# Performance work log

Measured on AMD Instinct MI355X. Metric: run time of the kernel, lower is better.

Reference implementation:

```python
import jax, jax.numpy as jnp
import numpy as np

B, D, E, H, T = 16384, 1024, 8, 512, 256
NUM_TASKS = 3  # purchase, quality, price


def setup_inputs() -> dict:
    key = jax.random.key(0)
    ks = jax.random.split(key, 12)
    s_in = 1.0 / np.sqrt(D)
    s_h = 1.0 / np.sqrt(H)
    s_t = 1.0 / np.sqrt(T)
    return {
        "x": jax.random.normal(ks[0], (B, D), dtype=jnp.float32),
        # expert layer 1: [E, D, H], layer 2: [E, H, H]
        "We1": jax.random.uniform(ks[1], (E, D, H), jnp.float32, -s_in, s_in),
        "be1": jax.random.uniform(ks[2], (E, H), jnp.float32, -s_in, s_in),
        "We2": jax.random.uniform(ks[3], (E, H, H), jnp.float32, -s_h, s_h),
        "be2": jax.random.uniform(ks[4], (E, H), jnp.float32, -s_h, s_h),
        # gates (one per task): [T_tasks, D, E]
        "Wg": jax.random.uniform(ks[5], (NUM_TASKS, D, E), jnp.float32, -s_in, s_in),
        "bg": jax.random.uniform(ks[6], (NUM_TASKS, E), jnp.float32, -s_in, s_in),
        # towers: [T_tasks, H, T] then [T_tasks, T, 1]
        "Wt1": jax.random.uniform(ks[7], (NUM_TASKS, H, T), jnp.float32, -s_h, s_h),
        "bt1": jax.random.uniform(ks[8], (NUM_TASKS, T), jnp.float32, -s_h, s_h),
        "Wt2": jax.random.uniform(ks[9], (NUM_TASKS, T, 1), jnp.float32, -s_t, s_t),
        "bt2": jax.random.uniform(ks[10], (NUM_TASKS, 1), jnp.float32, -s_t, s_t),
    }


def reference(x, We1, be1, We2, be2, Wg, bg, Wt1, bt1, Wt2, bt2):
    # Batched expert MLPs (dropout = identity in eval): [B, E, H]
    h1 = jax.nn.relu(jnp.einsum("bd,edh->beh", x, We1) + be1)
    expert_out = jax.nn.relu(jnp.einsum("beh,ehk->bek", h1, We2) + be2)
    # Per-task softmax gates: [T, B, E]
    gates = jax.nn.softmax(jnp.einsum("bd,tde->tbe", x, Wg) + bg[:, None, :], axis=-1)
    # Weighted combine: [T, B, H]
    task_in = jnp.einsum("tbe,beh->tbh", gates, expert_out)
    # Towers: [T, B, 1]
    th = jax.nn.relu(jnp.einsum("tbh,thk->tbk", task_in, Wt1) + bt1[:, None, :])
    preds = jax.nn.sigmoid(jnp.einsum("tbk,tko->tbo", th, Wt2) + bt2[:, None, :])
    return (preds[0], preds[1], preds[2])
```

## Files before the change

kernel.cpp:

```cpp
#include <hip/hip_runtime.h>


#define BM 128
#define BN 128
#define BK 64

typedef __attribute__((ext_vector_type(8))) short short8;
typedef __attribute__((ext_vector_type(4))) float floatx4;
typedef __attribute__((ext_vector_type(4))) unsigned short ushortx4;
typedef __attribute__((ext_vector_type(8))) unsigned short ushortx8;

__device__ __forceinline__ unsigned short f32_to_bf16(float f) {
  unsigned int u = __float_as_uint(f);
  u += 0x7fffu + ((u >> 16) & 1u);
  return (unsigned short)(u >> 16);
}
__device__ __forceinline__ float bf16_to_f32(unsigned short h) {
  return __uint_as_float(((unsigned int)h) << 16);
}

__device__ __forceinline__ void async_cp16(const void* g, void* lds) {
  __builtin_amdgcn_global_load_lds(
      (const __attribute__((address_space(1))) void*)g,
      (__attribute__((address_space(3))) void*)lds, 16, 0, 0);
}

__device__ __forceinline__ void transpose_slice(
    const float* __restrict__ in, unsigned short* __restrict__ out,
    int K, int N, float (*tile)[33]) {
  int n0 = blockIdx.x * 32, k0 = blockIdx.y * 32;
  for (int i = threadIdx.y; i < 32; i += 8)
    tile[i][threadIdx.x] = in[(size_t)(k0 + i) * N + n0 + threadIdx.x];
  __syncthreads();
  for (int i = threadIdx.y; i < 32; i += 8)
    out[(size_t)(n0 + i) * K + k0 + threadIdx.x] = f32_to_bf16(tile[threadIdx.x][i]);
}

__global__ void prep_kernel(const float* __restrict__ We1, const float* __restrict__ We2,
                            const float* __restrict__ Wt1, const float* __restrict__ Wg,
                            unsigned short* __restrict__ W1T, unsigned short* __restrict__ W2T,
                            unsigned short* __restrict__ Wt1T, float* __restrict__ WgT) {
  __shared__ float tile[32][33];
  int z = blockIdx.z;
  if (z < 8) {
    transpose_slice(We1 + (size_t)z * 524288, W1T + (size_t)z * 524288, 1024, 512, tile);
  } else if (z < 16) {
    if (blockIdx.y < 16)
      transpose_slice(We2 + (size_t)(z - 8) * 262144, W2T + (size_t)(z - 8) * 262144, 512, 512, tile);
  } else if (z < 19) {
    if (blockIdx.x < 8 && blockIdx.y < 16)
      transpose_slice(Wt1 + (size_t)(z - 16) * 131072, Wt1T + (size_t)(z - 16) * 131072, 512, 256, tile);
  } else {
    if (blockIdx.x < 16 && blockIdx.y < 6) {
      int idx = (blockIdx.y * 16 + blockIdx.x) * 256 + threadIdx.y * 32 + threadIdx.x;
      int t = idx >> 13, r = idx & 8191, e = r >> 10, d = r & 1023;
      WgT[idx] = Wg[t * 8192 + d * 8 + e];
    }
  }
}

__global__ __launch_bounds__(256) void gates_cvt_kernel(
    const float* __restrict__ x, const float* __restrict__ WgT,
    const float* __restrict__ bg, float* __restrict__ gout,
    unsigned short* __restrict__ xb) {
  int wave = threadIdx.x >> 6, lane = threadIdx.x & 63;
  int b = blockIdx.x * 4 + wave;
  const float* xr = x + (size_t)b * 1024;
  float xv[16];
#pragma unroll
  for (int j = 0; j < 16; j++) xv[j] = xr[lane + 64 * j];
  unsigned short* xbr = xb + (size_t)b * 1024;
#pragma unroll
  for (int j = 0; j < 16; j++) xbr[lane + 64 * j] = f32_to_bf16(xv[j]);
  float mylogit = 0.f;
#pragma unroll
  for (int te = 0; te < 24; te++) {
    const float* w = WgT + te * 1024;
    float a = 0.f;
#pragma unroll
    for (int j = 0; j < 16; j++) a += xv[j] * w[lane + 64 * j];
#pragma unroll
    for (int off = 32; off > 0; off >>= 1) a += __shfl_xor(a, off, 64);
    if (lane == te) mylogit = a;
  }
  if (lane < 24) {
    int t = lane >> 3, e = lane & 7;
    float logit = mylogit + bg[lane];
    float m = logit;
    m = fmaxf(m, __shfl_xor(m, 4, 64));
    m = fmaxf(m, __shfl_xor(m, 2, 64));
    m = fmaxf(m, __shfl_xor(m, 1, 64));
    float ex = __expf(logit - m);
    float s = ex;
    s += __shfl_xor(s, 4, 64);
    s += __shfl_xor(s, 2, 64);
    s += __shfl_xor(s, 1, 64);
    gout[(size_t)t * 131072 + (size_t)b * 8 + e] = ex / s;
  }
}

__global__ __launch_bounds__(256) void gemm_bt_relu(
    const unsigned short* __restrict__ Abase, long aOffZ, int lda,
    const unsigned short* __restrict__ Bbase, long bOffZ,
    const float* __restrict__ biasBase, int biasOffZ,
    unsigned short* __restrict__ Cbase, long cOffZ, int ldc,
    int K) {
  __shared__ __align__(16) unsigned short As[BM * BK];
  __shared__ __align__(16) unsigned short Bs[BN * BK];
  const int tid = threadIdx.x;
  const int z = blockIdx.z;
  const unsigned short* A = Abase + (size_t)aOffZ * z + (size_t)blockIdx.x * BM * lda;
  const unsigned short* Bt = Bbase + (size_t)bOffZ * z + (size_t)blockIdx.y * BN * K;
  const float* bias = biasBase + (size_t)biasOffZ * z + blockIdx.y * BN;
  unsigned short* C = Cbase + (size_t)cOffZ * z + (size_t)blockIdx.x * BM * ldc + blockIdx.y * BN;

  const int wave = tid >> 6, lane = tid & 63;
  const int wm = (wave >> 1) * 64, wn = (wave & 1) * 64;
  const int lm = lane & 15, lq = lane >> 4;
  const int sw = lm & 7;

  floatx4 acc[4][4] = {};

  const int sr = tid >> 3;
  const int sc = (((tid & 7) ^ (sr & 7)) << 3);

  for (int kt = 0; kt < K; kt += BK) {
#pragma unroll
    for (int i = 0; i < 4; i++)
      async_cp16(A + (size_t)(sr + 32 * i) * lda + kt + sc,
                 (char*)As + i * 4096 + tid * 16);
#pragma unroll
    for (int i = 0; i < 4; i++)
      async_cp16(Bt + (size_t)(sr + 32 * i) * K + kt + sc,
                 (char*)Bs + i * 4096 + tid * 16);
    __syncthreads();
#pragma unroll
    for (int ks = 0; ks < 2; ks++) {
      short8 af[4], bf[4];
      const int ch = ((ks * 4 + lq) ^ sw) << 3;
#pragma unroll
      for (int i = 0; i < 4; i++)
        af[i] = *(const short8*)(As + (wm + 16 * i + lm) * BK + ch);
#pragma unroll
      for (int j = 0; j < 4; j++)
        bf[j] = *(const short8*)(Bs + (wn + 16 * j + lm) * BK + ch);
#pragma unroll
      for (int i = 0; i < 4; i++)
#pragma unroll
        for (int j = 0; j < 4; j++)
          acc[i][j] = __builtin_amdgcn_mfma_f32_16x16x32_bf16(af[i], bf[j], acc[i][j], 0, 0, 0);
    }
    __syncthreads();
  }

#pragma unroll
  for (int i = 0; i < 4; i++) {
    const int row = wm + 16 * i + lq * 4;
#pragma unroll
    for (int j = 0; j < 4; j++) {
      const int col = wn + 16 * j + lm;
      const float bv = bias[col];
#pragma unroll
      for (int v = 0; v < 4; v++) {
        float val = fmaxf(acc[i][j][v] + bv, 0.0f);
        C[(size_t)(row + v) * ldc + col] = f32_to_bf16(val);
      }
    }
  }
}

__global__ __launch_bounds__(512) void tower_fused_kernel(
    const unsigned short* __restrict__ eoc, const float* __restrict__ gates,
    const unsigned short* __restrict__ Wt1T,
    const float* __restrict__ bt1, const float* __restrict__ Wt2,
    const float* __restrict__ bt2, float* __restrict__ out,
    int b0, int Bc) {
  __shared__ __align__(16) unsigned short As[128 * 64];
  __shared__ __align__(16) unsigned short Bs[256 * 64];
  const int tid = threadIdx.x;
  const int mtiles = Bc >> 7;
  const int t = blockIdx.x / mtiles;
  const int xbl = blockIdx.x % mtiles;
  const unsigned short* Bt = Wt1T + (size_t)t * 131072;

  const int wave = tid >> 6, lane = tid & 63;
  const int wm = (wave >> 2) * 64, wn = (wave & 3) * 64;
  const int lm = lane & 15, lq = lane >> 4;
  const int sw = lm & 7;

  floatx4 acc[4][4] = {};

  const int sr = tid >> 3;
  const int sc = (((tid & 7) ^ (sr & 7)) << 3);

  float gv[2][8];
#pragma unroll
  for (int r = 0; r < 2; r++) {
    const floatx4* gp = (const floatx4*)(
        gates + ((size_t)t * 16384 + b0 + (size_t)xbl * 128 + sr + 64 * r) * 8);
    floatx4 g0 = gp[0], g1 = gp[1];
#pragma unroll
    for (int j = 0; j < 4; j++) { gv[r][j] = g0[j]; gv[r][4 + j] = g1[j]; }
  }

  for (int kt = 0; kt < 512; kt += 64) {
#pragma unroll
    for (int r = 0; r < 2; r++) {
      const int bl = xbl * 128 + sr + 64 * r;
      float s[8] = {};
#pragma unroll
      for (int e = 0; e < 8; e++) {
        ushortx8 v = *(const ushortx8*)(eoc + ((size_t)bl * 8 + e) * 512 + kt + sc);
        const float g = gv[r][e];
#pragma unroll
        for (int j = 0; j < 8; j++) s[j] += g * bf16_to_f32(v[j]);
      }
      ushortx8 o;
#pragma unroll
      for (int j = 0; j < 8; j++) o[j] = f32_to_bf16(s[j]);
      *(ushortx8*)((char*)As + r * 8192 + tid * 16) = o;
    }
#pragma unroll
    for (int i = 0; i < 4; i++)
      async_cp16(Bt + (size_t)(sr + 64 * i) * 512 + kt + sc,
                 (char*)Bs + i * 8192 + tid * 16);
    __syncthreads();
#pragma unroll
    for (int ks = 0; ks < 2; ks++) {
      short8 af[4], bf[4];
      const int ch = ((ks * 4 + lq) ^ sw) << 3;
#pragma unroll
      for (int i = 0; i < 4; i++)
        af[i] = *(const short8*)(As + (wm + 16 * i + lm) * 64 + ch);
#pragma unroll
      for (int j = 0; j < 4; j++)
        bf[j] = *(const short8*)(Bs + (wn + 16 * j + lm) * 64 + ch);
#pragma unroll
      for (int i = 0; i < 4; i++)
#pragma unroll
        for (int j = 0; j < 4; j++)
          acc[i][j] = __builtin_amdgcn_mfma_f32_16x16x32_bf16(af[i], bf[j], acc[i][j], 0, 0, 0);
    }
    __syncthreads();
  }

  float b1v[4], w2v[4];
#pragma unroll
  for (int j = 0; j < 4; j++) {
    int col = wn + 16 * j + lm;
    b1v[j] = bt1[t * 256 + col];
    w2v[j] = Wt2[t * 256 + col];
  }
  float* pt = (float*)As;
#pragma unroll
  for (int i = 0; i < 4; i++) {
#pragma unroll
    for (int v = 0; v < 4; v++) {
      float p = 0.f;
#pragma unroll
      for (int j = 0; j < 4; j++)
        p += fmaxf(acc[i][j][v] + b1v[j], 0.0f) * w2v[j];
      p += __shfl_xor(p, 1, 64);
      p += __shfl_xor(p, 2, 64);
      p += __shfl_xor(p, 4, 64);
      p += __shfl_xor(p, 8, 64);
      if (lm == 0) pt[(wm + 16 * i + lq * 4 + v) * 4 + (wave & 3)] = p;
    }
  }
  __syncthreads();
  if (tid < 128) {
    float s = pt[tid * 4] + pt[tid * 4 + 1] + pt[tid * 4 + 2] + pt[tid * 4 + 3] + bt2[t];
    out[(t << 14) + b0 + xbl * 128 + tid] = 1.f / (1.f + __expf(-s));
  }
}

extern "C" void kernel_launch(void* const* d_in, const int* in_sizes, int n_in,
                              void* d_out, int out_size, void* d_ws, size_t ws_size,
                              hipStream_t stream) {
  (void)in_sizes; (void)n_in; (void)out_size;
  const float* x   = (const float*)d_in[0];
  const float* We1 = (const float*)d_in[1];
  const float* be1 = (const float*)d_in[2];
  const float* We2 = (const float*)d_in[3];
  const float* be2 = (const float*)d_in[4];
  const float* Wg  = (const float*)d_in[5];
  const float* bg  = (const float*)d_in[6];
  const float* Wt1 = (const float*)d_in[7];
  const float* bt1 = (const float*)d_in[8];
  const float* Wt2 = (const float*)d_in[9];
  const float* bt2 = (const float*)d_in[10];
  float* out = (float*)d_out;

  char* ws = (char*)d_ws;
  unsigned short* xb   = (unsigned short*)(ws + 0);
  unsigned short* W1T  = (unsigned short*)(ws + 33554432);
  unsigned short* W2T  = (unsigned short*)(ws + 41943040);
  unsigned short* Wt1T = (unsigned short*)(ws + 46137344);
  float*          gts  = (float*)(ws + 46923776);
  float*          WgT  = (float*)(ws + 48496640);
  const size_t fixed = 48594944;

  size_t rem = ws_size > fixed ? ws_size - fixed : 0;
  int Bc = 16384;
  while (Bc > 512 && (size_t)Bc * 16384 > rem) Bc >>= 1;
  const int nc = 16384 / Bc;

  char* cb = ws + fixed;
  unsigned short* h1c = (unsigned short*)(cb);
  unsigned short* eoc = (unsigned short*)(cb + (size_t)Bc * 8192);

  prep_kernel<<<dim3(16, 32, 20), dim3(32, 8), 0, stream>>>(We1, We2, Wt1, Wg, W1T, W2T, Wt1T, WgT);
  gates_cvt_kernel<<<4096, 256, 0, stream>>>(x, WgT, bg, gts, xb);

  for (int c = 0; c < nc; c++) {
    const unsigned short* xbc = xb + (size_t)c * Bc * 1024;
    gemm_bt_relu<<<dim3(Bc / 128, 4, 8), 256, 0, stream>>>(
        xbc, 0L, 1024, W1T, 524288L, be1, 512, h1c, 512L, 4096, 1024);
    gemm_bt_relu<<<dim3(Bc / 128, 4, 8), 256, 0, stream>>>(
        h1c, 512L, 4096, W2T, 262144L, be2, 512, eoc, 512L, 4096, 512);
    tower_fused_kernel<<<3 * (Bc / 128), 512, 0, stream>>>(
        eoc, gts, Wt1T, bt1, Wt2, bt2, out, c * Bc, Bc);
  }
}
```

Before: 525.5 us.

## Double-buffer tower kernel with 64-row tiles and register prefetch of expert outputs

Restructures the fused tower kernel to use 64-row M tiles with 256 threads (4 waves each covering 64 columns), doubling the grid size. Wt1 tiles are double-buffered in LDS and the next k-step's expert-output vectors are prefetched into registers, so the global loads overlap the MFMA work of the current step. One of the two barriers per iteration is replaced by a raw s_barrier wrapped in sched_barriers. The cost is more register pressure from the prefetch buffers, more LDS for the second B buffer, and each Wt1 tile being reloaded by twice as many blocks.

```diff
diff --git a/kernel.cpp b/kernel.cpp
--- a/kernel.cpp
+++ b/kernel.cpp
@@ -169,79 +169,98 @@
   }
 }
 
-__global__ __launch_bounds__(512) void tower_fused_kernel(
+__global__ __launch_bounds__(256, 2) void tower_fused_kernel(
     const unsigned short* __restrict__ eoc, const float* __restrict__ gates,
     const unsigned short* __restrict__ Wt1T,
     const float* __restrict__ bt1, const float* __restrict__ Wt2,
     const float* __restrict__ bt2, float* __restrict__ out,
     int b0, int Bc) {
-  __shared__ __align__(16) unsigned short As[128 * 64];
-  __shared__ __align__(16) unsigned short Bs[256 * 64];
+  __shared__ __align__(16) unsigned short As[64 * 64];
+  __shared__ __align__(16) unsigned short Bs[2][256 * 64];
   const int tid = threadIdx.x;
-  const int mtiles = Bc >> 7;
+  const int mtiles = Bc >> 6;
   const int t = blockIdx.x / mtiles;
   const int xbl = blockIdx.x % mtiles;
   const unsigned short* Bt = Wt1T + (size_t)t * 131072;
 
   const int wave = tid >> 6, lane = tid & 63;
-  const int wm = (wave >> 2) * 64, wn = (wave & 3) * 64;
+  const int wn = wave * 64;
   const int lm = lane & 15, lq = lane >> 4;
   const int sw = lm & 7;
-
-  floatx4 acc[4][4] = {};
-
   const int sr = tid >> 3;
   const int sc = (((tid & 7) ^ (sr & 7)) << 3);
 
+  floatx4 acc[4][4] = {};
+
   float gv[2][8];
 #pragma unroll
   for (int r = 0; r < 2; r++) {
     const floatx4* gp = (const floatx4*)(
-        gates + ((size_t)t * 16384 + b0 + (size_t)xbl * 128 + sr + 64 * r) * 8);
+        gates + ((size_t)t * 16384 + b0 + (size_t)xbl * 64 + sr + 32 * r) * 8);
     floatx4 g0 = gp[0], g1 = gp[1];
 #pragma unroll
     for (int j = 0; j < 4; j++) { gv[r][j] = g0[j]; gv[r][4 + j] = g1[j]; }
   }
 
+  const unsigned short* eb0 = eoc + ((size_t)(xbl * 64 + sr) * 8) * 512 + sc;
+  const unsigned short* eb1 = eoc + ((size_t)(xbl * 64 + sr + 32) * 8) * 512 + sc;
+
+  ushortx8 pv[2][8];
+
+#define STAGE_B_T(buf, kt_) do {                                             \
+    _Pragma("unroll") for (int i_ = 0; i_ < 8; ++i_)                         \
+      async_cp16(Bt + (size_t)(sr + 32 * i_) * 512 + (kt_) + sc,             \
+                 (char*)Bs[buf] + i_ * 4096 + tid * 16); } while (0)
+
+#define LOAD_PV(kt_) do {                                                    \
+    _Pragma("unroll") for (int e_ = 0; e_ < 8; ++e_) {                       \
+      pv[0][e_] = *(const ushortx8*)(eb0 + (size_t)e_ * 512 + (kt_));        \
+      pv[1][e_] = *(const ushortx8*)(eb1 + (size_t)e_ * 512 + (kt_));        \
+    } } while (0)
+
+  STAGE_B_T(0, 0);
+  LOAD_PV(0);
+
   for (int kt = 0; kt < 512; kt += 64) {
+    const int cur = (kt >> 6) & 1;
 #pragma unroll
     for (int r = 0; r < 2; r++) {
-      const int bl = xbl * 128 + sr + 64 * r;
       float s[8] = {};
 #pragma unroll
       for (int e = 0; e < 8; e++) {
-        ushortx8 v = *(const ushortx8*)(eoc + ((size_t)bl * 8 + e) * 512 + kt + sc);
         const float g = gv[r][e];
 #pragma unroll
-        for (int j = 0; j < 8; j++) s[j] += g * bf16_to_f32(v[j]);
+        for (int j = 0; j < 8; j++) s[j] += g * bf16_to_f32(pv[r][e][j]);
       }
       ushortx8 o;
 #pragma unroll
       for (int j = 0; j < 8; j++) o[j] = f32_to_bf16(s[j]);
-      *(ushortx8*)((char*)As + r * 8192 + tid * 16) = o;
-    }
-#pragma unroll
-    for (int i = 0; i < 4; i++)
-      async_cp16(Bt + (size_t)(sr + 64 * i) * 512 + kt + sc,
-                 (char*)Bs + i * 8192 + tid * 16);
+      *(ushortx8*)((char*)As + r * 4096 + tid * 16) = o;
+    }
     __syncthreads();
+    if (kt < 448) {
+      STAGE_B_T(cur ^ 1, kt + 64);
+      LOAD_PV(kt + 64);
+    }
 #pragma unroll
     for (int ks = 0; ks < 2; ks++) {
       short8 af[4], bf[4];
       const int ch = ((ks * 4 + lq) ^ sw) << 3;
 #pragma unroll
       for (int i = 0; i < 4; i++)
-        af[i] = *(const short8*)(As + (wm + 16 * i + lm) * 64 + ch);
+        af[i] = *(const short8*)(As + (16 * i + lm) * 64 + ch);
 #pragma unroll
       for (int j = 0; j < 4; j++)
-        bf[j] = *(const short8*)(Bs + (wn + 16 * j + lm) * 64 + ch);
+        bf[j] = *(const short8*)(Bs[cur] + (wn + 16 * j + lm) * 64 + ch);
 #pragma unroll
       for (int i = 0; i < 4; i++)
 #pragma unroll
         for (int j = 0; j < 4; j++)
           acc[i][j] = __builtin_amdgcn_mfma_f32_16x16x32_bf16(af[i], bf[j], acc[i][j], 0, 0, 0);
     }
-    __syncthreads();
+    __builtin_amdgcn_sched_barrier(0);
+    __builtin_amdgcn_s_barrier();
+    __builtin_amdgcn_sched_barrier(0);
   }
 
   float b1v[4], w2v[4];
@@ -264,13 +283,13 @@
       p += __shfl_xor(p, 2, 64);
       p += __shfl_xor(p, 4, 64);
       p += __shfl_xor(p, 8, 64);
-      if (lm == 0) pt[(wm + 16 * i + lq * 4 + v) * 4 + (wave & 3)] = p;
+      if (lm == 0) pt[(16 * i + lq * 4 + v) * 4 + wave] = p;
     }
   }
   __syncthreads();
-  if (tid < 128) {
+  if (tid < 64) {
     float s = pt[tid * 4] + pt[tid * 4 + 1] + pt[tid * 4 + 2] + pt[tid * 4 + 3] + bt2[t];
-    out[(t << 14) + b0 + xbl * 128 + tid] = 1.f / (1.f + __expf(-s));
+    out[(t << 14) + b0 + xbl * 64 + tid] = 1.f / (1.f + __expf(-s));
   }
 }
 
@@ -318,7 +337,7 @@
         xbc, 0L, 1024, W1T, 524288L, be1, 512, h1c, 512L, 4096, 1024);
     gemm_bt_relu<<<dim3(Bc / 128, 4, 8), 256, 0, stream>>>(
         h1c, 512L, 4096, W2T, 262144L, be2, 512, eoc, 512L, 4096, 512);
-    tower_fused_kernel<<<3 * (Bc / 128), 512, 0, stream>>>(
+    tower_fused_kernel<<<3 * (Bc / 64), 256, 0, stream>>>(
         eoc, gts, Wt1T, bt1, Wt2, bt2, out, c * Bc, Bc);
   }
 }
```

Measured after the change: 484.9 us, median of 3. 7.7% less time.
